# Optimization experiments

Measured on AMD Instinct MI355X. Metric: run time of the kernel, lower is better.

## Reference

```python
import functools
import jax, jax.numpy as jnp
import numpy as np

CUTOFF = 5.0
BOX = 80.0
N_POINTS = 8192
MAX_NEIGHBOURS = 32
MASK_VALUE = -1


def setup_inputs() -> dict:
    key = jax.random.key(0)
    positions = jax.random.uniform(key, (N_POINTS, 3), dtype=jnp.float32) * BOX
    return {"positions": positions, "max_neighbours": MAX_NEIGHBOURS}


def reference(positions, max_neighbours):
    # OpenBoundary.get_neighbours (include_self=False, cutoff=CUTOFF)
    n = positions.shape[0]
    # pairwise squared distances: vmap(neighbours_mask_direct) == full broadcast
    diff = positions[:, None, :] - positions[None, :, :]        # [N, N, 3]
    r2 = jnp.sum(diff * diff, axis=-1)                          # [N, N]
    neigh_mask = r2 <= CUTOFF * CUTOFF
    neigh_mask = neigh_mask & ~jnp.eye(n, dtype=bool)           # drop self
    # per-row compaction of hit indices into fixed-size buffer
    get_nb = functools.partial(jnp.argwhere, size=max_neighbours, fill_value=MASK_VALUE)
    to_idx = jax.vmap(get_nb)(neigh_mask)[..., 0]               # [N, max_neighbours]
    cell_indices = jnp.zeros((*to_idx.shape, 3), dtype=jnp.int32)
    actual_max_neighbours = jnp.max(neigh_mask.sum(axis=1))
    return to_idx, cell_indices, actual_max_neighbours
```

## Files before the change

### kernel.cpp

```cpp
#include <hip/hip_runtime.h>


constexpr int   N     = 8192;
constexpr int   MAXNB = 32;
constexpr float CUT2  = 25.0f;
constexpr int   C     = 15;
constexpr int   NCP   = 4096;
constexpr float INVW  = 0.1875f;
constexpr int   QBLOCKS = N / 4;

__device__ __forceinline__ int cell_coord(float v) {
    int c = (int)(v * INVW);
    return c > C - 1 ? C - 1 : c;
}

__global__ __launch_bounds__(1024) void build_kernel(const float* __restrict__ pos,
                                                     int* __restrict__ start_g,
                                                     float4* __restrict__ sorted) {
    __shared__ int cnt[NCP];
    __shared__ int wsum[16];
    const int t    = threadIdx.x;
    const int lane = t & 63;
    const int wv   = t >> 6;

    #pragma unroll
    for (int k = t; k < NCP; k += 1024) cnt[k] = 0;
    __syncthreads();

    float x[8], y[8], z[8];
    int cid[8], rnk[8];
    #pragma unroll
    for (int q = 0; q < 8; ++q) {
        const int i = q * 1024 + t;
        x[q] = pos[3 * i + 0];
        y[q] = pos[3 * i + 1];
        z[q] = pos[3 * i + 2];
        cid[q] = (cell_coord(z[q]) * C + cell_coord(y[q])) * C + cell_coord(x[q]);
        rnk[q] = atomicAdd(&cnt[cid[q]], 1);
    }
    __syncthreads();

    int c[4], pre[4], s0 = 0;
    #pragma unroll
    for (int k = 0; k < 4; ++k) { c[k] = cnt[4 * t + k]; pre[k] = s0; s0 += c[k]; }
    int inc = s0;
    #pragma unroll
    for (int off = 1; off < 64; off <<= 1) {
        const int v = __shfl_up(inc, off);
        if (lane >= off) inc += v;
    }
    if (lane == 63) wsum[wv] = inc;
    __syncthreads();
    if (t == 0) {
        int acc = 0;
        #pragma unroll
        for (int k = 0; k < 16; ++k) { const int tmp = wsum[k]; wsum[k] = acc; acc += tmp; }
    }
    __syncthreads();
    const int excl = wsum[wv] + (inc - s0);
    #pragma unroll
    for (int k = 0; k < 4; ++k) {
        cnt[4 * t + k]     = excl + pre[k];
        start_g[4 * t + k] = excl + pre[k];
    }
    if (t == 0) start_g[NCP] = N;
    __syncthreads();

    #pragma unroll
    for (int q = 0; q < 8; ++q) {
        const int p = cnt[cid[q]] + rnk[q];
        sorted[p] = make_float4(x[q], y[q], z[q], __int_as_float(q * 1024 + t));
    }
}

__global__ __launch_bounds__(256) void query_kernel(const float* __restrict__ pos,
                                                    const float4* __restrict__ sorted,
                                                    const int* __restrict__ start_g,
                                                    int* __restrict__ out_idx,
                                                    int* __restrict__ blockmax) {
    __shared__ int hitbuf[4][64];
    __shared__ int wmax[4];
    const int lane = threadIdx.x & 63;
    const int wave = threadIdx.x >> 6;
    const int p = __builtin_amdgcn_readfirstlane((int)blockIdx.x * 4 + wave);

    const float x = pos[3 * p + 0];
    const float y = pos[3 * p + 1];
    const float z = pos[3 * p + 2];
    const int cx = cell_coord(x), cy = cell_coord(y), cz = cell_coord(z);
    int xa = cx - 1; xa = xa < 0 ? 0 : (xa > C - 3 ? C - 3 : xa);
    int ya = cy - 1; ya = ya < 0 ? 0 : (ya > C - 3 ? C - 3 : ya);
    int za = cz - 1; za = za < 0 ? 0 : (za > C - 3 ? C - 3 : za);

    int bb[9], pre[10];
    pre[0] = 0;
    #pragma unroll
    for (int s = 0; s < 9; ++s) {
        const int rowb = ((za + s / 3) * C + (ya + s % 3)) * C + xa;
        bb[s] = start_g[rowb];
        pre[s + 1] = pre[s] + (start_g[rowb + 3] - bb[s]);
    }
    const int total = pre[9];

    int count = 0;
    for (int base = 0; base < total; base += 64) {
        const int l = base + lane;
        int idx = 0;
        #pragma unroll
        for (int s = 0; s < 9; ++s) {
            const bool in_s = (l >= pre[s]) && (l < pre[s + 1]);
            idx = in_s ? (bb[s] + (l - pre[s])) : idx;
        }
        const float4 o = sorted[idx];
        const float dx = __fsub_rn(x, o.x);
        const float dy = __fsub_rn(y, o.y);
        const float dz = __fsub_rn(z, o.z);
        const float r2 = __fadd_rn(__fadd_rn(__fmul_rn(dx, dx), __fmul_rn(dy, dy)),
                                   __fmul_rn(dz, dz));
        const int j = __float_as_int(o.w);
        const bool hit = (l < total) && (r2 <= CUT2) && (j != p);
        const unsigned long long m = __ballot(hit);
        if (hit) {
            const int pr = __builtin_amdgcn_mbcnt_hi(
                (unsigned int)(m >> 32),
                __builtin_amdgcn_mbcnt_lo((unsigned int)m, 0u));
            const int slot = count + pr;
            if (slot < 64) hitbuf[wave][slot] = j;
        }
        count += __popcll(m);
    }

    const int mcount = count < 64 ? count : 64;
    int v = (lane < mcount) ? hitbuf[wave][lane] : 0x7fffffff;
    #pragma unroll
    for (int k = 2; k <= 64; k <<= 1) {
        #pragma unroll
        for (int jj = k >> 1; jj >= 1; jj >>= 1) {
            const int pv = __shfl_xor(v, jj);
            const bool keepmin = ((lane & jj) == 0) == ((lane & k) == 0);
            v = keepmin ? min(v, pv) : max(v, pv);
        }
    }
    if (lane < MAXNB) out_idx[p * MAXNB + lane] = (lane < count) ? v : -1;

    if (lane == 0) wmax[wave] = count;
    __syncthreads();
    if (threadIdx.x == 0)
        blockmax[blockIdx.x] = max(max(wmax[0], wmax[1]), max(wmax[2], wmax[3]));
}

__global__ __launch_bounds__(256) void finalize_kernel(int4* __restrict__ cell4,
                                                       const int* __restrict__ blockmax,
                                                       int* __restrict__ out_max) {
    __shared__ int wm[4];
    const int idx = blockIdx.x * 256 + threadIdx.x;
    cell4[idx] = make_int4(0, 0, 0, 0);
    if (blockIdx.x == 0) {
        int mx = 0;
        for (int k = threadIdx.x; k < QBLOCKS; k += 256) mx = max(mx, blockmax[k]);
        #pragma unroll
        for (int off = 32; off > 0; off >>= 1) mx = max(mx, __shfl_down(mx, off));
        if ((threadIdx.x & 63) == 0) wm[threadIdx.x >> 6] = mx;
        __syncthreads();
        if (threadIdx.x == 0)
            *out_max = max(max(wm[0], wm[1]), max(wm[2], wm[3]));
    }
}

extern "C" void kernel_launch(void* const* d_in, const int* in_sizes, int n_in,
                              void* d_out, int out_size, void* d_ws, size_t ws_size,
                              hipStream_t stream) {
    const float* pos = (const float*)d_in[0];
    int* out = (int*)d_out;

    int* out_idx = out;
    int* base    = out + N * MAXNB;
    int* out_max = out + N * MAXNB * 4;

    int*    start_g  = base;
    float4* sorted   = (float4*)(base + 8192);
    int*    blockmax = (int*)d_ws;

    build_kernel   <<<1, 1024, 0, stream>>>(pos, start_g, sorted);
    query_kernel   <<<QBLOCKS, 256, 0, stream>>>(pos, sorted, start_g, out_idx, blockmax);
    finalize_kernel<<<N * MAXNB * 3 / 4 / 256, 256, 0, stream>>>((int4*)base, blockmax, out_max);
}
```

Baseline: 75.76 us.

## Fuse finalize into query kernel with atomic-counter max reduction and fast path

Removes the separate finalize kernel. The query kernel now zeroes the cell_indices output itself and computes the global max through a two-level last-block-done atomic reduction. The sort scratch moves from the output buffer into workspace. The cell grid changes to 16^3 with shift-based indexing, and a single-iteration fast path for candidate counts of 64 or fewer skips the LDS hit buffer. This saves one kernel launch and its tail, at the cost of atomics, workspace reliance, and slightly different cell binning.

New measurement: 113.4 us. 1.5x slower.

```diff
diff --git a/kernel.cpp b/kernel.cpp
--- a/kernel.cpp
+++ b/kernel.cpp
@@ -4,9 +4,9 @@
 constexpr int   N     = 8192;
 constexpr int   MAXNB = 32;
 constexpr float CUT2  = 25.0f;
-constexpr int   C     = 15;
-constexpr int   NCP   = 4096;
-constexpr float INVW  = 0.1875f;
+constexpr int   C     = 16;
+constexpr int   NCP   = C * C * C;
+constexpr float INVW  = 0.2f;
 constexpr int   QBLOCKS = N / 4;
 
 __device__ __forceinline__ int cell_coord(float v) {
@@ -16,13 +16,16 @@
 
 __global__ __launch_bounds__(1024) void build_kernel(const float* __restrict__ pos,
                                                      int* __restrict__ start_g,
-                                                     float4* __restrict__ sorted) {
+                                                     float4* __restrict__ sorted,
+                                                     int* __restrict__ done) {
     __shared__ int cnt[NCP];
     __shared__ int wsum[16];
     const int t    = threadIdx.x;
     const int lane = t & 63;
     const int wv   = t >> 6;
 
+    if (t < 33) done[t] = 0;
+
     #pragma unroll
     for (int k = t; k < NCP; k += 1024) cnt[k] = 0;
     __syncthreads();
@@ -35,7 +38,7 @@
         x[q] = pos[3 * i + 0];
         y[q] = pos[3 * i + 1];
         z[q] = pos[3 * i + 2];
-        cid[q] = (cell_coord(z[q]) * C + cell_coord(y[q])) * C + cell_coord(x[q]);
+        cid[q] = (cell_coord(z[q]) << 8) | (cell_coord(y[q]) << 4) | cell_coord(x[q]);
         rnk[q] = atomicAdd(&cnt[cid[q]], 1);
     }
     __syncthreads();
@@ -77,11 +80,19 @@
                                                     const float4* __restrict__ sorted,
                                                     const int* __restrict__ start_g,
                                                     int* __restrict__ out_idx,
-                                                    int* __restrict__ blockmax) {
+                                                    int4* __restrict__ cell4,
+                                                    int* __restrict__ blockmax,
+                                                    int* __restrict__ done1,
+                                                    int* __restrict__ done2,
+                                                    int* __restrict__ groupmax,
+                                                    int* __restrict__ out_max) {
     __shared__ int hitbuf[4][64];
     __shared__ int wmax[4];
     const int lane = threadIdx.x & 63;
     const int wave = threadIdx.x >> 6;
+
+    if (threadIdx.x < 96) cell4[blockIdx.x * 96 + threadIdx.x] = make_int4(0, 0, 0, 0);
+
     const int p = __builtin_amdgcn_readfirstlane((int)blockIdx.x * 4 + wave);
 
     const float x = pos[3 * p + 0];
@@ -96,20 +107,21 @@
     pre[0] = 0;
     #pragma unroll
     for (int s = 0; s < 9; ++s) {
-        const int rowb = ((za + s / 3) * C + (ya + s % 3)) * C + xa;
+        const int rowb = ((za + s / 3) << 8) + ((ya + s % 3) << 4) + xa;
         bb[s] = start_g[rowb];
         pre[s + 1] = pre[s] + (start_g[rowb + 3] - bb[s]);
     }
     const int total = pre[9];
 
     int count = 0;
-    for (int base = 0; base < total; base += 64) {
-        const int l = base + lane;
+    int v = 0x7fffffff;
+
+    if (total <= 64) {
         int idx = 0;
         #pragma unroll
         for (int s = 0; s < 9; ++s) {
-            const bool in_s = (l >= pre[s]) && (l < pre[s + 1]);
-            idx = in_s ? (bb[s] + (l - pre[s])) : idx;
+            const bool in_s = (lane >= pre[s]) && (lane < pre[s + 1]);
+            idx = in_s ? (bb[s] + (lane - pre[s])) : idx;
         }
         const float4 o = sorted[idx];
         const float dx = __fsub_rn(x, o.x);
@@ -118,20 +130,40 @@
         const float r2 = __fadd_rn(__fadd_rn(__fmul_rn(dx, dx), __fmul_rn(dy, dy)),
                                    __fmul_rn(dz, dz));
         const int j = __float_as_int(o.w);
-        const bool hit = (l < total) && (r2 <= CUT2) && (j != p);
-        const unsigned long long m = __ballot(hit);
-        if (hit) {
-            const int pr = __builtin_amdgcn_mbcnt_hi(
-                (unsigned int)(m >> 32),
-                __builtin_amdgcn_mbcnt_lo((unsigned int)m, 0u));
-            const int slot = count + pr;
-            if (slot < 64) hitbuf[wave][slot] = j;
-        }
-        count += __popcll(m);
-    }
-
-    const int mcount = count < 64 ? count : 64;
-    int v = (lane < mcount) ? hitbuf[wave][lane] : 0x7fffffff;
+        const bool hit = (lane < total) && (r2 <= CUT2) && (j != p);
+        count = __popcll(__ballot(hit));
+        v = hit ? j : 0x7fffffff;
+    } else {
+        for (int base = 0; base < total; base += 64) {
+            const int l = base + lane;
+            int idx = 0;
+            #pragma unroll
+            for (int s = 0; s < 9; ++s) {
+                const bool in_s = (l >= pre[s]) && (l < pre[s + 1]);
+                idx = in_s ? (bb[s] + (l - pre[s])) : idx;
+            }
+            const float4 o = sorted[idx];
+            const float dx = __fsub_rn(x, o.x);
+            const float dy = __fsub_rn(y, o.y);
+            const float dz = __fsub_rn(z, o.z);
+            const float r2 = __fadd_rn(__fadd_rn(__fmul_rn(dx, dx), __fmul_rn(dy, dy)),
+                                       __fmul_rn(dz, dz));
+            const int j = __float_as_int(o.w);
+            const bool hit = (l < total) && (r2 <= CUT2) && (j != p);
+            const unsigned long long m = __ballot(hit);
+            if (hit) {
+                const int pr = __builtin_amdgcn_mbcnt_hi(
+                    (unsigned int)(m >> 32),
+                    __builtin_amdgcn_mbcnt_lo((unsigned int)m, 0u));
+                const int slot = count + pr;
+                if (slot < 64) hitbuf[wave][slot] = j;
+            }
+            count += __popcll(m);
+        }
+        const int mcount = count < 64 ? count : 64;
+        v = (lane < mcount) ? hitbuf[wave][lane] : 0x7fffffff;
+    }
+
     #pragma unroll
     for (int k = 2; k <= 64; k <<= 1) {
         #pragma unroll
@@ -145,25 +177,37 @@
 
     if (lane == 0) wmax[wave] = count;
     __syncthreads();
-    if (threadIdx.x == 0)
-        blockmax[blockIdx.x] = max(max(wmax[0], wmax[1]), max(wmax[2], wmax[3]));
-}
-
-__global__ __launch_bounds__(256) void finalize_kernel(int4* __restrict__ cell4,
-                                                       const int* __restrict__ blockmax,
-                                                       int* __restrict__ out_max) {
-    __shared__ int wm[4];
-    const int idx = blockIdx.x * 256 + threadIdx.x;
-    cell4[idx] = make_int4(0, 0, 0, 0);
-    if (blockIdx.x == 0) {
-        int mx = 0;
-        for (int k = threadIdx.x; k < QBLOCKS; k += 256) mx = max(mx, blockmax[k]);
-        #pragma unroll
-        for (int off = 32; off > 0; off >>= 1) mx = max(mx, __shfl_down(mx, off));
-        if ((threadIdx.x & 63) == 0) wm[threadIdx.x >> 6] = mx;
-        __syncthreads();
-        if (threadIdx.x == 0)
-            *out_max = max(max(wm[0], wm[1]), max(wm[2], wm[3]));
+
+    if (wave == 0) {
+        const int b = (int)blockIdx.x;
+        const int g = b >> 6;
+        const int bmax = max(max(wmax[0], wmax[1]), max(wmax[2], wmax[3]));
+        int old = 0;
+        if (lane == 0) {
+            __hip_atomic_store(&blockmax[b], bmax, __ATOMIC_RELAXED, __HIP_MEMORY_SCOPE_AGENT);
+            old = __hip_atomic_fetch_add(&done1[g], 1, __ATOMIC_ACQ_REL, __HIP_MEMORY_SCOPE_AGENT);
+        }
+        old = __shfl(old, 0);
+        if (old == 63) {
+            int gm = __hip_atomic_load(&blockmax[(g << 6) + lane],
+                                       __ATOMIC_RELAXED, __HIP_MEMORY_SCOPE_AGENT);
+            #pragma unroll
+            for (int off = 32; off > 0; off >>= 1) gm = max(gm, __shfl_xor(gm, off));
+            int old2 = 0;
+            if (lane == 0) {
+                __hip_atomic_store(&groupmax[g], gm, __ATOMIC_RELAXED, __HIP_MEMORY_SCOPE_AGENT);
+                old2 = __hip_atomic_fetch_add(done2, 1, __ATOMIC_ACQ_REL, __HIP_MEMORY_SCOPE_AGENT);
+            }
+            old2 = __shfl(old2, 0);
+            if (old2 == 31) {
+                int m2 = (lane < 32)
+                    ? __hip_atomic_load(&groupmax[lane], __ATOMIC_RELAXED, __HIP_MEMORY_SCOPE_AGENT)
+                    : 0;
+                #pragma unroll
+                for (int off = 32; off > 0; off >>= 1) m2 = max(m2, __shfl_xor(m2, off));
+                if (lane == 0) *out_max = m2;
+            }
+        }
     }
 }
 
@@ -173,15 +217,18 @@
     const float* pos = (const float*)d_in[0];
     int* out = (int*)d_out;
 
-    int* out_idx = out;
-    int* base    = out + N * MAXNB;
-    int* out_max = out + N * MAXNB * 4;
-
-    int*    start_g  = base;
-    float4* sorted   = (float4*)(base + 8192);
-    int*    blockmax = (int*)d_ws;
-
-    build_kernel   <<<1, 1024, 0, stream>>>(pos, start_g, sorted);
-    query_kernel   <<<QBLOCKS, 256, 0, stream>>>(pos, sorted, start_g, out_idx, blockmax);
-    finalize_kernel<<<N * MAXNB * 3 / 4 / 256, 256, 0, stream>>>((int4*)base, blockmax, out_max);
-}
+    int*  out_idx = out;
+    int4* cell4   = (int4*)(out + N * MAXNB);
+    int*  out_max = out + N * MAXNB * 4;
+
+    char*   ws       = (char*)d_ws;
+    float4* sorted   = (float4*)ws;
+    int*    start_g  = (int*)(ws + 131072);
+    int*    blockmax = (int*)(ws + 147968);
+    int*    groupmax = (int*)(ws + 156160);
+    int*    done     = (int*)(ws + 156288);
+
+    build_kernel<<<1, 1024, 0, stream>>>(pos, start_g, sorted, done);
+    query_kernel<<<QBLOCKS, 256, 0, stream>>>(pos, sorted, start_g, out_idx, cell4,
+                                              blockmax, done, done + 32, groupmax, out_max);
+}
```
